# Performance work log

Hardware: AMD Instinct MI355X
Metric: run time of the kernel (lower is better)

Reference implementation:

```python
import jax, jax.numpy as jnp
import numpy as np

N_GRAPHS = 256

def setup_inputs() -> dict:
    key = jax.random.key(0)
    ks = jax.random.split(key, 8)
    N, E, C, H, L, O = 50000, 800000, 128, 128, 3, 1
    s = 1.0 / np.sqrt(H)
    x = jax.random.normal(ks[0], (N, C), jnp.float32)
    edge_index = jax.random.randint(ks[1], (2, E), 0, N)
    batch = jnp.sort(jax.random.randint(ks[2], (N,), 0, N_GRAPHS))
    W1 = jax.random.normal(ks[3], (L, C, H), jnp.float32) * s
    b1 = jnp.zeros((L, H), jnp.float32)
    W2 = jax.random.normal(ks[4], (L, H, H), jnp.float32) * s
    b2 = jnp.zeros((L, H), jnp.float32)
    eps = jnp.zeros((L,), jnp.float32)
    Wh = jax.random.normal(ks[5], (H, O), jnp.float32) * s
    bh = jnp.zeros((O,), jnp.float32)
    return dict(x=x, edge_index=edge_index, batch=batch, W1=W1, b1=b1,
                W2=W2, b2=b2, eps=eps, Wh=Wh, bh=bh)

def reference(x, edge_index, batch, W1, b1, W2, b2, eps, Wh, bh):
    # GIN (PyG BasicGNN, norm=None): per layer h = MLP((1+eps)*h + sum_{j->i} h_j),
    # MLP = Linear -> ReLU -> Linear; ReLU (+dropout, identity at eval) between layers.
    src, dst = edge_index[0], edge_index[1]
    N = x.shape[0]
    L = W1.shape[0]
    h = x
    for l in range(L):
        agg = jax.ops.segment_sum(h[src], dst, num_segments=N)   # [N, H] scatter-add
        z = (1.0 + eps[l]) * h + agg
        z = jnp.maximum(z @ W1[l] + b1[l], 0.0) @ W2[l] + b2[l]
        h = jnp.maximum(z, 0.0) if l < L - 1 else z
    # global_mean_pool over graph ids
    sums = jax.ops.segment_sum(h, batch, num_segments=N_GRAPHS)
    cnt = jax.ops.segment_sum(jnp.ones((N,), h.dtype), batch, num_segments=N_GRAPHS)
    pooled = sums / jnp.maximum(cnt, 1.0)[:, None]               # [G, H]
    return pooled @ Wh + bh                                      # [G, out_channels]
```

## Files before the change

### kernel.cpp

```cpp
#include <hip/hip_runtime.h>
#include <cstdint>

#define H 128
#define NGRAPH 256
#define ROWSTRIDE 68
#define NPB 256
#define CSR_CAP 6144
#define SCHUNK 4096

typedef __attribute__((ext_vector_type(8))) short short8;
typedef __attribute__((ext_vector_type(4))) float floatx4;

typedef unsigned short u16;
typedef unsigned int u32;

__device__ __forceinline__ u16 f2b(float f) {
    union { float f; u32 u; } v; v.f = f;
    u32 r = v.u + 0x7fffu + ((v.u >> 16) & 1u);
    return (u16)(r >> 16);
}
__device__ __forceinline__ float b2f(u16 b) {
    union { u32 u; float f; } v; v.u = ((u32)b) << 16;
    return v.f;
}
__device__ __forceinline__ float lo_f(u32 v) {
    union { u32 u; float f; } w; w.u = v << 16; return w.f;
}
__device__ __forceinline__ float hi_f(u32 v) {
    union { u32 u; float f; } w; w.u = v & 0xffff0000u; return w.f;
}

__global__ __launch_bounds__(256) void prep_kernel(const float* __restrict__ x,
                                                   u16* __restrict__ xb,
                                                   const float* __restrict__ W1,
                                                   const float* __restrict__ W2,
                                                   u16* __restrict__ packed,
                                                   const int* __restrict__ dstv,
                                                   int* __restrict__ bcnt,
                                                   int n4, int total, int E, int NB,
                                                   int nConv, int nPack) {
    __shared__ int sh[256];
    const int t = threadIdx.x;
    const int b = blockIdx.x;
    if (b < nConv) {
        int i = b * 256 + t;
        if (i < n4) {
            float4 v = *(const float4*)(x + (size_t)i * 4);
            u16 o[4] = { f2b(v.x), f2b(v.y), f2b(v.z), f2b(v.w) };
            *(uint2*)(xb + (size_t)i * 4) = *(uint2*)o;
        }
    } else if (b < nConv + nPack) {
        int idx = (b - nConv) * 256 + t;
        if (idx < total) {
            int mat = idx >> 14;
            int pos = idx & 16383;
            int j    = pos & 7;
            int lane = (pos >> 3) & 63;
            int nt   = (pos >> 9) & 7;
            int kc   = pos >> 12;
            int k = kc * 32 + (lane >> 4) * 8 + j;
            int n = nt * 16 + (lane & 15);
            const float* src = (mat < 3) ? (W1 + (size_t)mat * H * H)
                                         : (W2 + (size_t)(mat - 3) * H * H);
            packed[idx] = f2b(src[(size_t)k * H + n]);
        }
    } else {
        int bb = b - nConv - nPack;
        sh[t] = 0;
        __syncthreads();
        for (int e = bb * 256 + t; e < E; e += 256 * 256)
            atomicAdd(&sh[dstv[e] >> 8], 1);
        __syncthreads();
        if (t < NB && sh[t] > 0) atomicAdd(&bcnt[t], sh[t]);
    }
}

__global__ __launch_bounds__(256) void scatter_kernel(const int* __restrict__ src,
                                                      const int* __restrict__ dstv,
                                                      const int* __restrict__ bcnt,
                                                      int* __restrict__ bcursor,
                                                      u32* __restrict__ stage, int E, int NB) {
    __shared__ int lcnt[256];
    __shared__ int lbase[256];
    __shared__ int sA[256];
    __shared__ int sB[256];
    int t = threadIdx.x;
    int v = (t < NB) ? bcnt[t] : 0;
    sA[t] = v;
    lcnt[t] = 0;
    __syncthreads();
    int* a = sA; int* bb2 = sB;
    for (int off = 1; off < 256; off <<= 1) {
        bb2[t] = (t >= off) ? (a[t] + a[t - off]) : a[t];
        __syncthreads();
        int* tmp = a; a = bb2; bb2 = tmp;
    }
    bb2[t] = a[t] - v;
    __syncthreads();

    int base = blockIdx.x * SCHUNK;
    u32 pk[16];
    int bk[16];
#pragma unroll
    for (int i = 0; i < 16; ++i) {
        int idx = base + t + i * 256;
        bk[i] = -1;
        if (idx < E) {
            int s = src[idx];
            int d = dstv[idx];
            int b = d >> 8;
            pk[i] = (u32)s | ((u32)(d & 255) << 24);
            bk[i] = b;
            atomicAdd(&lcnt[b], 1);
        }
    }
    __syncthreads();
    if (t < NB && lcnt[t] > 0) lbase[t] = sB[t] + atomicAdd(&bcursor[t], lcnt[t]);
    __syncthreads();
    lcnt[t] = 0;
    __syncthreads();
#pragma unroll
    for (int i = 0; i < 16; ++i) {
        if (bk[i] >= 0) {
            int r = atomicAdd(&lcnt[bk[i]], 1);
            stage[(size_t)lbase[bk[i]] + r] = pk[i];
        }
    }
}

__global__ __launch_bounds__(256) void build_csr(const u32* __restrict__ stage,
                                                 const int* __restrict__ bcnt,
                                                 int* __restrict__ offs, int* __restrict__ cols,
                                                 int N, int NB, int E) {
    __shared__ int cnt[256];
    __shared__ int cur[256];
    __shared__ int sA[256];
    __shared__ int sB[256];
    __shared__ int colstage[CSR_CAP];
    int b = blockIdx.x;
    int t = threadIdx.x;
    int v = (t < NB) ? bcnt[t] : 0;
    sA[t] = v;
    __syncthreads();
    int* a = sA; int* bb2 = sB;
    for (int off = 1; off < 256; off <<= 1) {
        bb2[t] = (t >= off) ? (a[t] + a[t - off]) : a[t];
        __syncthreads();
        int* tmp = a; a = bb2; bb2 = tmp;
    }
    int lo = (b == 0) ? 0 : a[b - 1];
    int hi = a[b];
    __syncthreads();
    int sz = hi - lo;
    int nlo = b * NPB;
    cnt[t] = 0;
    __syncthreads();
    for (int i = t; i < sz; i += 256) atomicAdd(&cnt[stage[(size_t)lo + i] >> 24], 1);
    __syncthreads();
    sA[t] = cnt[t];
    __syncthreads();
    a = sA; bb2 = sB;
    for (int off = 1; off < 256; off <<= 1) {
        bb2[t] = (t >= off) ? (a[t] + a[t - off]) : a[t];
        __syncthreads();
        int* tmp = a; a = bb2; bb2 = tmp;
    }
    int excl = a[t] - cnt[t];
    if (nlo + t < N) offs[nlo + t] = lo + excl;
    if (b == 0 && t == 0) offs[N] = E;
    cur[t] = excl;
    __syncthreads();
    if (sz <= CSR_CAP) {
        for (int i = t; i < sz; i += 256) {
            u32 pk = stage[(size_t)lo + i];
            int r = atomicAdd(&cur[pk >> 24], 1);
            colstage[r] = (int)(pk & 0xFFFFFFu);
        }
        __syncthreads();
        for (int i = t; i < sz; i += 256) cols[(size_t)lo + i] = colstage[i];
    } else {
        for (int i = t; i < sz; i += 256) {
            u32 pk = stage[(size_t)lo + i];
            int r = atomicAdd(&cur[pk >> 24], 1);
            cols[(size_t)lo + r] = (int)(pk & 0xFFFFFFu);
        }
    }
}

__global__ __launch_bounds__(256) void fused_layer(const u16* __restrict__ h,
                                                   u16* __restrict__ hout,
                                                   const int* __restrict__ offs,
                                                   const int* __restrict__ cols,
                                                   const u16* __restrict__ Wp1,
                                                   const u16* __restrict__ Wp2,
                                                   const float* __restrict__ bias1,
                                                   const float* __restrict__ bias2,
                                                   const float* __restrict__ eps, int layer,
                                                   int relu2, int lastLayer,
                                                   const float* __restrict__ Wh,
                                                   float* __restrict__ y, int N) {
    __shared__ u32 ldsA[16 * ROWSTRIDE];
    __shared__ u32 ldsB[16 * ROWSTRIDE];
    __shared__ float dacc[16];

    const int tid = threadIdx.x;
    const int wave = tid >> 6;
    const int lane = tid & 63;
    const int m = lane & 15;
    const int quad = lane >> 4;
    const int nt0 = wave * 2, nt1 = wave * 2 + 1;
    const int row0 = blockIdx.x * 16;

    const float scale = 1.0f + eps[layer];
    const u32* __restrict__ hp = (const u32*)h;

    {
        const int nid = wave * 4 + quad;
        const int node = row0 + nid;
        float a[8];
#pragma unroll
        for (int i = 0; i < 8; ++i) a[i] = 0.f;
        if (node < N) {
#pragma unroll
            for (int i = 0; i < 4; ++i) {
                u32 v = hp[(size_t)node * 64 + m + 16 * i];
                a[2 * i]     = scale * lo_f(v);
                a[2 * i + 1] = scale * hi_f(v);
            }
            int beg = offs[node], end = offs[node + 1];
            int j = beg;
            for (; j + 4 <= end; j += 4) {
                int c0 = cols[j], c1 = cols[j + 1], c2 = cols[j + 2], c3 = cols[j + 3];
                u32 v0[4], v1[4], v2[4], v3[4];
#pragma unroll
                for (int i = 0; i < 4; ++i) v0[i] = hp[(size_t)c0 * 64 + m + 16 * i];
#pragma unroll
                for (int i = 0; i < 4; ++i) v1[i] = hp[(size_t)c1 * 64 + m + 16 * i];
#pragma unroll
                for (int i = 0; i < 4; ++i) v2[i] = hp[(size_t)c2 * 64 + m + 16 * i];
#pragma unroll
                for (int i = 0; i < 4; ++i) v3[i] = hp[(size_t)c3 * 64 + m + 16 * i];
#pragma unroll
                for (int i = 0; i < 4; ++i) {
                    a[2 * i]     += (lo_f(v0[i]) + lo_f(v1[i])) + (lo_f(v2[i]) + lo_f(v3[i]));
                    a[2 * i + 1] += (hi_f(v0[i]) + hi_f(v1[i])) + (hi_f(v2[i]) + hi_f(v3[i]));
                }
            }
            for (; j < end; ++j) {
                int c0 = cols[j];
#pragma unroll
                for (int i = 0; i < 4; ++i) {
                    u32 v = hp[(size_t)c0 * 64 + m + 16 * i];
                    a[2 * i]     += lo_f(v);
                    a[2 * i + 1] += hi_f(v);
                }
            }
        }
#pragma unroll
        for (int i = 0; i < 4; ++i) {
            u16 p[2] = { f2b(a[2 * i]), f2b(a[2 * i + 1]) };
            ldsA[nid * ROWSTRIDE + m + 16 * i] = *(u32*)p;
        }
    }

    short8 B1f0[4], B1f1[4], B2f0[4], B2f1[4];
#pragma unroll
    for (int kc = 0; kc < 4; ++kc) {
        B1f0[kc] = *(const short8*)(Wp1 + ((size_t)(kc * 8 + nt0) * 64 + lane) * 8);
        B1f1[kc] = *(const short8*)(Wp1 + ((size_t)(kc * 8 + nt1) * 64 + lane) * 8);
        B2f0[kc] = *(const short8*)(Wp2 + ((size_t)(kc * 8 + nt0) * 64 + lane) * 8);
        B2f1[kc] = *(const short8*)(Wp2 + ((size_t)(kc * 8 + nt1) * 64 + lane) * 8);
    }
    const int cg0 = nt0 * 16 + m, cg1 = nt1 * 16 + m;
    const float b1v0 = bias1[cg0], b1v1 = bias1[cg1];
    const float b2v0 = bias2[cg0], b2v1 = bias2[cg1];
    __syncthreads();

    {
        short8 a0 = *(const short8*)(&ldsA[m * ROWSTRIDE + 0 * 16 + quad * 4]);
        short8 a1 = *(const short8*)(&ldsA[m * ROWSTRIDE + 1 * 16 + quad * 4]);
        short8 a2 = *(const short8*)(&ldsA[m * ROWSTRIDE + 2 * 16 + quad * 4]);
        short8 a3 = *(const short8*)(&ldsA[m * ROWSTRIDE + 3 * 16 + quad * 4]);
        floatx4 acc0 = {0.f, 0.f, 0.f, 0.f};
        floatx4 acc1 = {0.f, 0.f, 0.f, 0.f};
        acc0 = __builtin_amdgcn_mfma_f32_16x16x32_bf16(a0, B1f0[0], acc0, 0, 0, 0);
        acc1 = __builtin_amdgcn_mfma_f32_16x16x32_bf16(a0, B1f1[0], acc1, 0, 0, 0);
        acc0 = __builtin_amdgcn_mfma_f32_16x16x32_bf16(a1, B1f0[1], acc0, 0, 0, 0);
        acc1 = __builtin_amdgcn_mfma_f32_16x16x32_bf16(a1, B1f1[1], acc1, 0, 0, 0);
        acc0 = __builtin_amdgcn_mfma_f32_16x16x32_bf16(a2, B1f0[2], acc0, 0, 0, 0);
        acc1 = __builtin_amdgcn_mfma_f32_16x16x32_bf16(a2, B1f1[2], acc1, 0, 0, 0);
        acc0 = __builtin_amdgcn_mfma_f32_16x16x32_bf16(a3, B1f0[3], acc0, 0, 0, 0);
        acc1 = __builtin_amdgcn_mfma_f32_16x16x32_bf16(a3, B1f1[3], acc1, 0, 0, 0);
        u16* lb = (u16*)ldsB;
#pragma unroll
        for (int i = 0; i < 4; ++i) {
            int rr = quad * 4 + i;
            lb[rr * (ROWSTRIDE * 2) + cg0] = f2b(fmaxf(acc0[i] + b1v0, 0.f));
            lb[rr * (ROWSTRIDE * 2) + cg1] = f2b(fmaxf(acc1[i] + b1v1, 0.f));
        }
        if (tid < 16) dacc[tid] = 0.f;
    }
    __syncthreads();

    {
        short8 a0 = *(const short8*)(&ldsB[m * ROWSTRIDE + 0 * 16 + quad * 4]);
        short8 a1 = *(const short8*)(&ldsB[m * ROWSTRIDE + 1 * 16 + quad * 4]);
        short8 a2 = *(const short8*)(&ldsB[m * ROWSTRIDE + 2 * 16 + quad * 4]);
        short8 a3 = *(const short8*)(&ldsB[m * ROWSTRIDE + 3 * 16 + quad * 4]);
        floatx4 acc0 = {0.f, 0.f, 0.f, 0.f};
        floatx4 acc1 = {0.f, 0.f, 0.f, 0.f};
        acc0 = __builtin_amdgcn_mfma_f32_16x16x32_bf16(a0, B2f0[0], acc0, 0, 0, 0);
        acc1 = __builtin_amdgcn_mfma_f32_16x16x32_bf16(a0, B2f1[0], acc1, 0, 0, 0);
        acc0 = __builtin_amdgcn_mfma_f32_16x16x32_bf16(a1, B2f0[1], acc0, 0, 0, 0);
        acc1 = __builtin_amdgcn_mfma_f32_16x16x32_bf16(a1, B2f1[1], acc1, 0, 0, 0);
        acc0 = __builtin_amdgcn_mfma_f32_16x16x32_bf16(a2, B2f0[2], acc0, 0, 0, 0);
        acc1 = __builtin_amdgcn_mfma_f32_16x16x32_bf16(a2, B2f1[2], acc1, 0, 0, 0);
        acc0 = __builtin_amdgcn_mfma_f32_16x16x32_bf16(a3, B2f0[3], acc0, 0, 0, 0);
        acc1 = __builtin_amdgcn_mfma_f32_16x16x32_bf16(a3, B2f1[3], acc1, 0, 0, 0);

        if (!lastLayer) {
            u16* la = (u16*)ldsA;
#pragma unroll
            for (int i = 0; i < 4; ++i) {
                int rr = quad * 4 + i;
                float v0 = acc0[i] + b2v0;
                float v1 = acc1[i] + b2v1;
                if (relu2) { v0 = fmaxf(v0, 0.f); v1 = fmaxf(v1, 0.f); }
                la[rr * (ROWSTRIDE * 2) + cg0] = f2b(v0);
                la[rr * (ROWSTRIDE * 2) + cg1] = f2b(v1);
            }
            __syncthreads();
            int rr = tid >> 4;
            int s  = tid & 15;
            int grow = row0 + rr;
            if (grow < N) {
                uint4 v = *(uint4*)(&ldsA[rr * ROWSTRIDE + s * 4]);
                *(uint4*)(hout + (size_t)grow * H + s * 8) = v;
            }
        } else {
            const float wh0 = Wh[cg0], wh1 = Wh[cg1];
            float part[4];
#pragma unroll
            for (int i = 0; i < 4; ++i)
                part[i] = b2f(f2b(acc0[i] + b2v0)) * wh0 +
                          b2f(f2b(acc1[i] + b2v1)) * wh1;
#pragma unroll
            for (int off = 1; off < 16; off <<= 1)
#pragma unroll
                for (int i = 0; i < 4; ++i) part[i] += __shfl_xor(part[i], off, 64);
            if (m == 0) {
#pragma unroll
                for (int i = 0; i < 4; ++i) atomicAdd(&dacc[quad * 4 + i], part[i]);
            }
            __syncthreads();
            if (tid < 16 && row0 + tid < N) y[row0 + tid] = dacc[tid];
        }
    }
}

__device__ __forceinline__ int lbound(const int* __restrict__ a, int n, int v) {
    int lo = 0, hi = n;
    while (lo < hi) { int mid = (lo + hi) >> 1; if (a[mid] < v) lo = mid + 1; else hi = mid; }
    return lo;
}

__global__ void seg_out_kernel(const float* __restrict__ y, const int* __restrict__ batch,
                               const float* __restrict__ bh, float* __restrict__ out, int N) {
    __shared__ float sh[256];
    int g = blockIdx.x;
    int lo = lbound(batch, N, g);
    int hi = lbound(batch, N, g + 1);
    float s = 0.f;
    for (int i = lo + threadIdx.x; i < hi; i += 256) s += y[i];
    sh[threadIdx.x] = s;
    __syncthreads();
    for (int off = 128; off > 0; off >>= 1) {
        if (threadIdx.x < off) sh[threadIdx.x] += sh[threadIdx.x + off];
        __syncthreads();
    }
    if (threadIdx.x == 0) {
        float cnt = (float)(hi - lo);
        out[g] = sh[0] / fmaxf(cnt, 1.0f) + bh[0];
    }
}

extern "C" void kernel_launch(void* const* d_in, const int* in_sizes, int n_in,
                              void* d_out, int out_size, void* d_ws, size_t ws_size,
                              hipStream_t stream) {
    const float* x    = (const float*)d_in[0];
    const int*   eidx = (const int*)d_in[1];
    const int*   batch= (const int*)d_in[2];
    const float* W1   = (const float*)d_in[3];
    const float* b1   = (const float*)d_in[4];
    const float* W2   = (const float*)d_in[5];
    const float* b2   = (const float*)d_in[6];
    const float* eps  = (const float*)d_in[7];
    const float* Wh   = (const float*)d_in[8];
    const float* bh   = (const float*)d_in[9];

    const int N = in_sizes[0] / H;
    const int E = in_sizes[1] / 2;
    const int L = in_sizes[7];
    const int* src  = eidx;
    const int* dstv = eidx + E;
    float* out = (float*)d_out;

    const int NB = (N + NPB - 1) / NPB;

    char* w = (char*)d_ws;
    u16* B0 = (u16*)w; w += (size_t)N * H * sizeof(u16);
    u16* B1 = (u16*)w; w += (size_t)N * H * sizeof(u16);
    u16* packedW = (u16*)w; w += (size_t)6 * H * H * sizeof(u16);
    float* y    = (float*)w; w += (size_t)N * sizeof(float);
    int* offs   = (int*)w;   w += (size_t)(N + 1) * sizeof(int);
    int* bcnt   = (int*)w;   w += 256 * sizeof(int);
    int* bcursor= (int*)w;   w += 256 * sizeof(int);
    u32* stage  = (u32*)w;   w += (size_t)E * sizeof(u32);
    int* cols   = (int*)w;   w += (size_t)E * sizeof(int);

    hipMemsetAsync(bcnt, 0, 512 * sizeof(int), stream);

    const int n4 = N * H / 4;
    const int total = 6 * H * H;
    const int nConv = (n4 + 255) / 256;
    const int nPack = (total + 255) / 256;
    prep_kernel<<<nConv + nPack + 256, 256, 0, stream>>>(x, B0, W1, W2, packedW,
                                                         dstv, bcnt, n4, total, E, NB,
                                                         nConv, nPack);

    scatter_kernel<<<(E + SCHUNK - 1) / SCHUNK, 256, 0, stream>>>(src, dstv, bcnt, bcursor,
                                                                  stage, E, NB);
    build_csr<<<NB, 256, 0, stream>>>(stage, bcnt, offs, cols, N, NB, E);

    const int numTiles = (N + 15) / 16;
    u16* bufs[2] = { B0, B1 };
    int cur = 0;
    for (int l = 0; l < L; ++l) {
        int nxt = cur ^ 1;
        int last = (l == L - 1) ? 1 : 0;
        fused_layer<<<numTiles, 256, 0, stream>>>(bufs[cur], bufs[nxt], offs, cols,
                                                  packedW + (size_t)l * H * H,
                                                  packedW + (size_t)(3 + l) * H * H,
                                                  b1 + (size_t)l * H, b2 + (size_t)l * H,
                                                  eps, l, (l < L - 1) ? 1 : 0, last,
                                                  Wh, y, N);
        cur = nxt;
    }

    seg_out_kernel<<<NGRAPH, 256, 0, stream>>>(y, batch, bh, out, N);
}
```

Baseline: 245.4 us.

## Enlarge fused GIN layer tile to 32 nodes with 8 waves per block

The fused layer kernel now processes 32 nodes per block with 512 threads. Each of the 8 waves owns a single 16-column output tile and runs two 16-row MFMAs per k-chunk instead of two column tiles for 16 rows. This halves per-wave weight fragment registers and halves the total weight-fragment global loads across the grid, at the cost of larger blocks and more LDS per block. The gather, store and final-layer reduction paths are adjusted to index the extra 16 rows.

```diff
diff --git a/kernel.cpp b/kernel.cpp
--- a/kernel.cpp
+++ b/kernel.cpp
@@ -187,7 +187,7 @@
     }
 }
 
-__global__ __launch_bounds__(256) void fused_layer(const u16* __restrict__ h,
+__global__ __launch_bounds__(512) void fused_layer(const u16* __restrict__ h,
                                                    u16* __restrict__ hout,
                                                    const int* __restrict__ offs,
                                                    const int* __restrict__ cols,
@@ -199,17 +199,17 @@
                                                    int relu2, int lastLayer,
                                                    const float* __restrict__ Wh,
                                                    float* __restrict__ y, int N) {
-    __shared__ u32 ldsA[16 * ROWSTRIDE];
-    __shared__ u32 ldsB[16 * ROWSTRIDE];
-    __shared__ float dacc[16];
+    __shared__ u32 ldsA[32 * ROWSTRIDE];
+    __shared__ u32 ldsB[32 * ROWSTRIDE];
+    __shared__ float dacc[32];
 
     const int tid = threadIdx.x;
     const int wave = tid >> 6;
     const int lane = tid & 63;
     const int m = lane & 15;
     const int quad = lane >> 4;
-    const int nt0 = wave * 2, nt1 = wave * 2 + 1;
-    const int row0 = blockIdx.x * 16;
+    const int nt = wave;
+    const int row0 = blockIdx.x * 32;
 
     const float scale = 1.0f + eps[layer];
     const u32* __restrict__ hp = (const u32*)h;
@@ -263,71 +263,59 @@
         }
     }
 
-    short8 B1f0[4], B1f1[4], B2f0[4], B2f1[4];
+    short8 B1f[4], B2f[4];
 #pragma unroll
     for (int kc = 0; kc < 4; ++kc) {
-        B1f0[kc] = *(const short8*)(Wp1 + ((size_t)(kc * 8 + nt0) * 64 + lane) * 8);
-        B1f1[kc] = *(const short8*)(Wp1 + ((size_t)(kc * 8 + nt1) * 64 + lane) * 8);
-        B2f0[kc] = *(const short8*)(Wp2 + ((size_t)(kc * 8 + nt0) * 64 + lane) * 8);
-        B2f1[kc] = *(const short8*)(Wp2 + ((size_t)(kc * 8 + nt1) * 64 + lane) * 8);
-    }
-    const int cg0 = nt0 * 16 + m, cg1 = nt1 * 16 + m;
-    const float b1v0 = bias1[cg0], b1v1 = bias1[cg1];
-    const float b2v0 = bias2[cg0], b2v1 = bias2[cg1];
+        B1f[kc] = *(const short8*)(Wp1 + ((size_t)(kc * 8 + nt) * 64 + lane) * 8);
+        B2f[kc] = *(const short8*)(Wp2 + ((size_t)(kc * 8 + nt) * 64 + lane) * 8);
+    }
+    const int cg = nt * 16 + m;
+    const float b1v = bias1[cg];
+    const float b2v = bias2[cg];
+    if (tid < 32) dacc[tid] = 0.f;
     __syncthreads();
 
     {
-        short8 a0 = *(const short8*)(&ldsA[m * ROWSTRIDE + 0 * 16 + quad * 4]);
-        short8 a1 = *(const short8*)(&ldsA[m * ROWSTRIDE + 1 * 16 + quad * 4]);
-        short8 a2 = *(const short8*)(&ldsA[m * ROWSTRIDE + 2 * 16 + quad * 4]);
-        short8 a3 = *(const short8*)(&ldsA[m * ROWSTRIDE + 3 * 16 + quad * 4]);
         floatx4 acc0 = {0.f, 0.f, 0.f, 0.f};
         floatx4 acc1 = {0.f, 0.f, 0.f, 0.f};
-        acc0 = __builtin_amdgcn_mfma_f32_16x16x32_bf16(a0, B1f0[0], acc0, 0, 0, 0);
-        acc1 = __builtin_amdgcn_mfma_f32_16x16x32_bf16(a0, B1f1[0], acc1, 0, 0, 0);
-        acc0 = __builtin_amdgcn_mfma_f32_16x16x32_bf16(a1, B1f0[1], acc0, 0, 0, 0);
-        acc1 = __builtin_amdgcn_mfma_f32_16x16x32_bf16(a1, B1f1[1], acc1, 0, 0, 0);
-        acc0 = __builtin_amdgcn_mfma_f32_16x16x32_bf16(a2, B1f0[2], acc0, 0, 0, 0);
-        acc1 = __builtin_amdgcn_mfma_f32_16x16x32_bf16(a2, B1f1[2], acc1, 0, 0, 0);
-        acc0 = __builtin_amdgcn_mfma_f32_16x16x32_bf16(a3, B1f0[3], acc0, 0, 0, 0);
-        acc1 = __builtin_amdgcn_mfma_f32_16x16x32_bf16(a3, B1f1[3], acc1, 0, 0, 0);
+#pragma unroll
+        for (int kc = 0; kc < 4; ++kc) {
+            short8 a0 = *(const short8*)(&ldsA[(0 + m) * ROWSTRIDE + kc * 16 + quad * 4]);
+            short8 a1 = *(const short8*)(&ldsA[(16 + m) * ROWSTRIDE + kc * 16 + quad * 4]);
+            acc0 = __builtin_amdgcn_mfma_f32_16x16x32_bf16(a0, B1f[kc], acc0, 0, 0, 0);
+            acc1 = __builtin_amdgcn_mfma_f32_16x16x32_bf16(a1, B1f[kc], acc1, 0, 0, 0);
+        }
         u16* lb = (u16*)ldsB;
 #pragma unroll
         for (int i = 0; i < 4; ++i) {
             int rr = quad * 4 + i;
-            lb[rr * (ROWSTRIDE * 2) + cg0] = f2b(fmaxf(acc0[i] + b1v0, 0.f));
-            lb[rr * (ROWSTRIDE * 2) + cg1] = f2b(fmaxf(acc1[i] + b1v1, 0.f));
-        }
-        if (tid < 16) dacc[tid] = 0.f;
+            lb[rr * (ROWSTRIDE * 2) + cg]        = f2b(fmaxf(acc0[i] + b1v, 0.f));
+            lb[(16 + rr) * (ROWSTRIDE * 2) + cg] = f2b(fmaxf(acc1[i] + b1v, 0.f));
+        }
     }
     __syncthreads();
 
     {
-        short8 a0 = *(const short8*)(&ldsB[m * ROWSTRIDE + 0 * 16 + quad * 4]);
-        short8 a1 = *(const short8*)(&ldsB[m * ROWSTRIDE + 1 * 16 + quad * 4]);
-        short8 a2 = *(const short8*)(&ldsB[m * ROWSTRIDE + 2 * 16 + quad * 4]);
-        short8 a3 = *(const short8*)(&ldsB[m * ROWSTRIDE + 3 * 16 + quad * 4]);
         floatx4 acc0 = {0.f, 0.f, 0.f, 0.f};
         floatx4 acc1 = {0.f, 0.f, 0.f, 0.f};
-        acc0 = __builtin_amdgcn_mfma_f32_16x16x32_bf16(a0, B2f0[0], acc0, 0, 0, 0);
-        acc1 = __builtin_amdgcn_mfma_f32_16x16x32_bf16(a0, B2f1[0], acc1, 0, 0, 0);
-        acc0 = __builtin_amdgcn_mfma_f32_16x16x32_bf16(a1, B2f0[1], acc0, 0, 0, 0);
-        acc1 = __builtin_amdgcn_mfma_f32_16x16x32_bf16(a1, B2f1[1], acc1, 0, 0, 0);
-        acc0 = __builtin_amdgcn_mfma_f32_16x16x32_bf16(a2, B2f0[2], acc0, 0, 0, 0);
-        acc1 = __builtin_amdgcn_mfma_f32_16x16x32_bf16(a2, B2f1[2], acc1, 0, 0, 0);
-        acc0 = __builtin_amdgcn_mfma_f32_16x16x32_bf16(a3, B2f0[3], acc0, 0, 0, 0);
-        acc1 = __builtin_amdgcn_mfma_f32_16x16x32_bf16(a3, B2f1[3], acc1, 0, 0, 0);
+#pragma unroll
+        for (int kc = 0; kc < 4; ++kc) {
+            short8 a0 = *(const short8*)(&ldsB[(0 + m) * ROWSTRIDE + kc * 16 + quad * 4]);
+            short8 a1 = *(const short8*)(&ldsB[(16 + m) * ROWSTRIDE + kc * 16 + quad * 4]);
+            acc0 = __builtin_amdgcn_mfma_f32_16x16x32_bf16(a0, B2f[kc], acc0, 0, 0, 0);
+            acc1 = __builtin_amdgcn_mfma_f32_16x16x32_bf16(a1, B2f[kc], acc1, 0, 0, 0);
+        }
 
         if (!lastLayer) {
             u16* la = (u16*)ldsA;
 #pragma unroll
             for (int i = 0; i < 4; ++i) {
                 int rr = quad * 4 + i;
-                float v0 = acc0[i] + b2v0;
-                float v1 = acc1[i] + b2v1;
+                float v0 = acc0[i] + b2v;
+                float v1 = acc1[i] + b2v;
                 if (relu2) { v0 = fmaxf(v0, 0.f); v1 = fmaxf(v1, 0.f); }
-                la[rr * (ROWSTRIDE * 2) + cg0] = f2b(v0);
-                la[rr * (ROWSTRIDE * 2) + cg1] = f2b(v1);
+                la[rr * (ROWSTRIDE * 2) + cg]        = f2b(v0);
+                la[(16 + rr) * (ROWSTRIDE * 2) + cg] = f2b(v1);
             }
             __syncthreads();
             int rr = tid >> 4;
@@ -338,22 +326,29 @@
                 *(uint4*)(hout + (size_t)grow * H + s * 8) = v;
             }
         } else {
-            const float wh0 = Wh[cg0], wh1 = Wh[cg1];
-            float part[4];
-#pragma unroll
-            for (int i = 0; i < 4; ++i)
-                part[i] = b2f(f2b(acc0[i] + b2v0)) * wh0 +
-                          b2f(f2b(acc1[i] + b2v1)) * wh1;
+            const float wh = Wh[cg];
+            float p0[4], p1[4];
+#pragma unroll
+            for (int i = 0; i < 4; ++i) {
+                p0[i] = b2f(f2b(acc0[i] + b2v)) * wh;
+                p1[i] = b2f(f2b(acc1[i] + b2v)) * wh;
+            }
 #pragma unroll
             for (int off = 1; off < 16; off <<= 1)
 #pragma unroll
-                for (int i = 0; i < 4; ++i) part[i] += __shfl_xor(part[i], off, 64);
+                for (int i = 0; i < 4; ++i) {
+                    p0[i] += __shfl_xor(p0[i], off, 64);
+                    p1[i] += __shfl_xor(p1[i], off, 64);
+                }
             if (m == 0) {
 #pragma unroll
-                for (int i = 0; i < 4; ++i) atomicAdd(&dacc[quad * 4 + i], part[i]);
+                for (int i = 0; i < 4; ++i) {
+                    atomicAdd(&dacc[quad * 4 + i], p0[i]);
+                    atomicAdd(&dacc[16 + quad * 4 + i], p1[i]);
+                }
             }
             __syncthreads();
-            if (tid < 16 && row0 + tid < N) y[row0 + tid] = dacc[tid];
+            if (tid < 32 && row0 + tid < N) y[row0 + tid] = dacc[tid];
         }
     }
 }
@@ -432,13 +427,13 @@
                                                                   stage, E, NB);
     build_csr<<<NB, 256, 0, stream>>>(stage, bcnt, offs, cols, N, NB, E);
 
-    const int numTiles = (N + 15) / 16;
+    const int numTiles = (N + 31) / 32;
     u16* bufs[2] = { B0, B1 };
     int cur = 0;
     for (int l = 0; l < L; ++l) {
         int nxt = cur ^ 1;
         int last = (l == L - 1) ? 1 : 0;
-        fused_layer<<<numTiles, 256, 0, stream>>>(bufs[cur], bufs[nxt], offs, cols,
+        fused_layer<<<numTiles, 512, 0, stream>>>(bufs[cur], bufs[nxt], offs, cols,
                                                   packedW + (size_t)l * H * H,
                                                   packedW + (size_t)(3 + l) * H * H,
                                                   b1 + (size_t)l * H, b2 + (size_t)l * H,
```

Result: faster. 236.9 us (median of 2 runs) (-3.5%).
